# Performance work log

Hardware: AMD Instinct MI355X
Metric: run time of the kernel (lower is better)

Reference implementation:

```python
import jax, jax.numpy as jnp
import numpy as np

MAXLEN = 100  # target_node_incoming_edge_maxlim in to_dense_batch_JY


def setup_inputs() -> dict:
    key = jax.random.key(0)
    ks = jax.random.split(key, 6)
    N, F, H, B = 500000, 64, 64, 8192
    x = jax.random.normal(ks[0], (N, F), dtype=jnp.float32)
    index = jnp.sort(jax.random.randint(ks[1], (N,), 0, B)).astype(jnp.int64)
    s = 1.0 / np.sqrt(H)  # torch LSTM reset_parameters: U(-1/sqrt(H), 1/sqrt(H))
    W_ih = jax.random.uniform(ks[2], (4 * H, F), jnp.float32, -s, s)
    W_hh = jax.random.uniform(ks[3], (4 * H, H), jnp.float32, -s, s)
    b_ih = jax.random.uniform(ks[4], (4 * H,), jnp.float32, -s, s)
    b_hh = jax.random.uniform(ks[5], (4 * H,), jnp.float32, -s, s)
    return {"x": x, "W_ih": W_ih, "W_hh": W_hh, "b_ih": b_ih, "b_hh": b_hh,
            "index": index, "dim_size": B}


def _lstm_last_hidden(dense, mask, W_ih, W_hh, b_ih, b_hh):
    """Run a single-layer LSTM over dense [B,L,F]; freeze state where mask is
    False, which reproduces pack_sequence semantics (ht = hidden at last valid
    step of each sequence; zero-length sequences stay at h0=0)."""
    B, L, F = dense.shape
    H = W_hh.shape[1]
    # input projection for all timesteps at once: [B, L, 4H]
    xg = jnp.einsum('blf,gf->blg', dense, W_ih) + (b_ih + b_hh)

    def step(carry, inp):
        h, c = carry
        g_x, m = inp                      # g_x: [B,4H], m: [B] bool
        g = g_x + h @ W_hh.T
        i, f, gc, o = jnp.split(g, 4, axis=-1)  # torch gate order: i, f, g, o
        i = jax.nn.sigmoid(i)
        f = jax.nn.sigmoid(f)
        gc = jnp.tanh(gc)
        o = jax.nn.sigmoid(o)
        c_new = f * c + i * gc
        h_new = o * jnp.tanh(c_new)
        m2 = m[:, None]
        return (jnp.where(m2, h_new, h), jnp.where(m2, c_new, c)), None

    h0 = jnp.zeros((B, H), dense.dtype)
    (h, _c), _ = jax.lax.scan(step, (h0, h0),
                              (jnp.swapaxes(xg, 0, 1), mask.T))
    return h  # [B, H] == ht[-1]


def reference(x, W_ih, W_hh, b_ih, b_hh, index, dim_size):
    N, F = x.shape
    index = index.astype(jnp.int32)
    # per-graph node counts and exclusive-cumsum offsets (index is sorted)
    counts = jax.ops.segment_sum(jnp.ones(N, jnp.int32), index,
                                 num_segments=dim_size)
    offsets = jnp.concatenate([jnp.zeros(1, jnp.int32),
                               jnp.cumsum(counts)[:-1].astype(jnp.int32)])
    pos = jnp.arange(N, dtype=jnp.int32) - offsets[index]  # position in graph
    valid = pos < MAXLEN                                   # truncate to 100
    # scatter into dense [B, MAXLEN, F]; invalid rows are zeroed and added at
    # slot 0 so they are no-ops
    dense = jnp.zeros((dim_size, MAXLEN, F), x.dtype)
    dense = dense.at[index, jnp.where(valid, pos, 0)].add(
        jnp.where(valid[:, None], x, 0.0))
    seq_len = jnp.minimum(counts, MAXLEN)
    mask = jnp.arange(MAXLEN)[None, :] < seq_len[:, None]  # [B, MAXLEN]
    return _lstm_last_hidden(dense, mask, W_ih, W_hh, b_ih, b_hh)
```

## Files before the change

kernel.cpp:

```cpp
#include <hip/hip_runtime.h>

#define MAXLEN 100
#define HDIM 64
#define CH 4
#define NSEG 12
#define SROW 72
#define SPLANE (CH * SROW + 8)
#define HSTR 72
#define L2E 1.44269504f

typedef __attribute__((ext_vector_type(8))) short bf16x8;
typedef __attribute__((ext_vector_type(4))) float f32x4;

#define LGKM_BARRIER() asm volatile("s_waitcnt lgkmcnt(0)\n\ts_barrier" ::: "memory")

__device__ __forceinline__ unsigned cvtpk(float a, float b) {
    unsigned r;
    asm("v_cvt_pk_bf16_f32 %0, %1, %2" : "=v"(r) : "v"(a), "v"(b));
    return r;
}
__device__ __forceinline__ bf16x8 pack8(f32x4 a, f32x4 b) {
    union { unsigned u[4]; bf16x8 v; } c;
    c.u[0] = cvtpk(a[0], a[1]); c.u[1] = cvtpk(a[2], a[3]);
    c.u[2] = cvtpk(b[0], b[1]); c.u[3] = cvtpk(b[2], b[3]);
    return c.v;
}
__device__ __forceinline__ float sig_pre(float a) {
    return __builtin_amdgcn_rcpf(1.0f + __builtin_amdgcn_exp2f(a));
}
__device__ __forceinline__ float tanh_pre(float a) {
    return fmaf(2.0f, __builtin_amdgcn_rcpf(1.0f + __builtin_amdgcn_exp2f(a)), -1.0f);
}
__device__ __forceinline__ float tanh_p(float v) {
    return fmaf(2.0f, __builtin_amdgcn_rcpf(1.0f + __builtin_amdgcn_exp2f(v * (-2.0f * L2E))), -1.0f);
}

__global__ void seg_hist_kernel(const int* __restrict__ index,
                                int* __restrict__ segStart,
                                int* __restrict__ hist, int N, int B) {
    const int s = blockIdx.x * blockDim.x + threadIdx.x;
    if (s > B) return;
    int lo = 0, hi = N;
    while (lo < hi) { int m = (lo + hi) >> 1; if (index[m] < s) lo = m + 1; else hi = m; }
    segStart[s] = lo;
    if (s < B) {
        int l2 = lo, h2 = N;
        while (l2 < h2) { int m = (l2 + h2) >> 1; if (index[m] < s + 1) l2 = m + 1; else h2 = m; }
        int len = l2 - lo;
        len = len < MAXLEN ? len : MAXLEN;
        atomicAdd(&hist[len], 1);
    }
}

__global__ void seg_scatter_kernel(const int* __restrict__ segStart,
                                   const int* __restrict__ hist,
                                   int* __restrict__ cnt,
                                   int2* __restrict__ slotPacked,
                                   int B, int nslots) {
    __shared__ int base_s[MAXLEN + 1];
    const int tid = threadIdx.x;
    __shared__ int hist_s[MAXLEN + 1];
    if (tid <= MAXLEN) hist_s[tid] = hist[tid];
    __syncthreads();
    if (tid == 0) {
        int acc = 0;
        for (int l = MAXLEN; l >= 0; --l) { base_s[l] = acc; acc += hist_s[l]; }
    }
    __syncthreads();
    const int stride = gridDim.x * blockDim.x;
    for (int b = blockIdx.x * blockDim.x + tid; b < B; b += stride) {
        const int s0 = segStart[b];
        int len = segStart[b + 1] - s0;
        len = len < MAXLEN ? len : MAXLEN;
        const int slot = base_s[len] + atomicAdd(&cnt[len], 1);
        slotPacked[slot] = make_int2(s0, (b << 7) | len);
    }
    if (blockIdx.x == 0 && tid < nslots - B) slotPacked[B + tid] = make_int2(0, -128);
}

__global__ __launch_bounds__(256, 3)
void lstm12_kernel(const float* __restrict__ x,
                   const float* __restrict__ Wih,
                   const float* __restrict__ Whh,
                   const float* __restrict__ bih,
                   const float* __restrict__ bhh,
                   const int* __restrict__ index,
                   const int2* __restrict__ slotPacked,
                   float* __restrict__ out, int N, int B) {
    const int tid  = threadIdx.x;
    const int w    = tid >> 6;
    const int lane = tid & 63;
    const int l15  = lane & 15;
    const int quad = lane >> 4;
    const int segbase = blockIdx.x * NSEG;
    const int ncol = w * 16 + l15;

    __shared__ __align__(16) unsigned short xst[NSEG * SPLANE];
    __shared__ __align__(16) unsigned short hst[2][16][HSTR];
    __shared__ int sstart[NSEG], slen[NSEG], sseg[NSEG];

    if (tid < NSEG) {
        const int slot = segbase + tid;
        int sg = -1, s = 0, len = 0;
        if (slotPacked != nullptr) {
            const int2 p = slotPacked[slot];
            s   = p.x;
            sg  = p.y >> 7;
            len = p.y & 127;
        } else {
            const int b = slot;
            if (b < B) {
                sg = b;
                int lo = 0, hi = N;
                while (lo < hi) { int m = (lo + hi) >> 1; if (index[m] < b) lo = m + 1; else hi = m; }
                s = lo;
                hi = N;
                while (lo < hi) { int m = (lo + hi) >> 1; if (index[m] < b + 1) lo = m + 1; else hi = m; }
                len = lo - s;
                len = len < MAXLEN ? len : MAXLEN;
            }
        }
        sstart[tid] = s;
        slen[tid] = len;
        sseg[tid] = sg;
    }
    for (int i = tid; i < 2 * 16 * HSTR / 2; i += 256) ((int*)hst)[i] = 0;
    __syncthreads();

    bf16x8 wi[4][2], wh[4][2];
    f32x4 bsv[4];
#pragma unroll
    for (int g = 0; g < 4; ++g) {
        const float sc = (g == 2) ? (-2.0f * L2E) : (-L2E);
        const int row = g * HDIM + ncol;
        const float bb = sc * (bih[row] + bhh[row]);
        bsv[g][0] = bb; bsv[g][1] = bb; bsv[g][2] = bb; bsv[g][3] = bb;
#pragma unroll
        for (int kt = 0; kt < 2; ++kt) {
            const f32x4* pi = (const f32x4*)(Wih + (size_t)row * HDIM + kt * 32 + quad * 8);
            const f32x4* ph = (const f32x4*)(Whh + (size_t)row * HDIM + kt * 32 + quad * 8);
            wi[g][kt] = pack8(pi[0] * sc, pi[1] * sc);
            wh[g][kt] = pack8(ph[0] * sc, ph[1] * sc);
        }
    }

    int len3[3];
#pragma unroll
    for (int r = 0; r < 3; ++r) len3[r] = slen[quad * 3 + r];
    int lmax = 0;
#pragma unroll
    for (int i = 0; i < NSEG; ++i) { int v = slen[i]; lmax = v > lmax ? v : lmax; }
    lmax = __builtin_amdgcn_readfirstlane(lmax);

    const int sS = tid >> 4, sT = (tid >> 2) & 3, sC = tid & 3;
    const int sst = (tid < 192) ? sstart[sS] : 0;
    const int sln = (tid < 192) ? slen[sS] : 0;

    f32x4 pre[4];

#define ISSUE(t0_)                                                              \
    if (w < 3) {                                                                \
        int ct = (t0_) + sT;                                                    \
        ct = (sln > 0) ? (ct < sln ? ct : sln - 1) : 0;                         \
        int row = sst + ct;                                                     \
        row = row < N - 1 ? row : N - 1;                                        \
        const f32x4* p_ = (const f32x4*)(x + (size_t)row * HDIM + sC * 16);     \
        pre[0] = p_[0]; pre[1] = p_[1]; pre[2] = p_[2]; pre[3] = p_[3];         \
    }
#define COMMIT()                                                                \
    if (w < 3) {                                                                \
        uint4 o1, o2;                                                           \
        o1.x = cvtpk(pre[0][0], pre[0][1]); o1.y = cvtpk(pre[0][2], pre[0][3]); \
        o1.z = cvtpk(pre[1][0], pre[1][1]); o1.w = cvtpk(pre[1][2], pre[1][3]); \
        o2.x = cvtpk(pre[2][0], pre[2][1]); o2.y = cvtpk(pre[2][2], pre[2][3]); \
        o2.z = cvtpk(pre[3][0], pre[3][1]); o2.w = cvtpk(pre[3][2], pre[3][3]); \
        unsigned short* d_ = &xst[sS * SPLANE + sT * SROW + sC * 16];           \
        *(uint4*)d_ = o1; *(uint4*)(d_ + 8) = o2;                               \
    }

    const int m3 = l15 & 3;
    const int xp = (l15 >> 2) * 3 + (m3 < 2 ? m3 : 2);
    const unsigned short* xb = &xst[xp * SPLANE + quad * 8];

    f32x4 accx[4];
#define ACCX(tt_)                                                               \
    {                                                                           \
        const unsigned short* xr_ = xb + (tt_) * SROW;                          \
        bf16x8 xa0_ = *(const bf16x8*)(xr_);                                    \
        bf16x8 xa1_ = *(const bf16x8*)(xr_ + 32);                               \
        _Pragma("unroll")                                                       \
        for (int g_ = 0; g_ < 4; ++g_) {                                        \
            f32x4 a_ = __builtin_amdgcn_mfma_f32_16x16x32_bf16(xa0_, wi[g_][0], bsv[g_], 0, 0, 0); \
            accx[g_] = __builtin_amdgcn_mfma_f32_16x16x32_bf16(xa1_, wi[g_][1], a_, 0, 0, 0); \
        }                                                                       \
    }

    float c3[3] = {0, 0, 0}, h3[3] = {0, 0, 0};
    const int nch = (lmax + CH - 1) / CH;

    if (nch > 0) {
        ISSUE(0);
        COMMIT();
        LGKM_BARRIER();
        ACCX(0);
        if (nch > 1) ISSUE(CH);

        for (int ch = 0; ch < nch; ++ch) {
            const int t0 = ch * CH;
#pragma unroll
            for (int tt = 0; tt < CH; ++tt) {
                const int t = t0 + tt;
                const int pb = tt & 1, nb = pb ^ 1;

                const unsigned short* hr = &hst[pb][l15][quad * 8];
                bf16x8 ha0 = *(const bf16x8*)(hr);
                bf16x8 ha1 = *(const bf16x8*)(hr + 32);

                f32x4 acc[4];
#pragma unroll
                for (int g = 0; g < 4; ++g) {
                    f32x4 a = __builtin_amdgcn_mfma_f32_16x16x32_bf16(ha0, wh[g][0], accx[g], 0, 0, 0);
                    acc[g] = __builtin_amdgcn_mfma_f32_16x16x32_bf16(ha1, wh[g][1], a, 0, 0, 0);
                }

                if (tt + 1 < CH) ACCX(tt + 1);

#pragma unroll
                for (int r = 0; r < 3; ++r) {
                    float gi = sig_pre (acc[0][r]);
                    float gf = sig_pre (acc[1][r]);
                    float gg = tanh_pre(acc[2][r]);
                    float go = sig_pre (acc[3][r]);
                    float cn = fmaf(gf, c3[r], gi * gg);
                    float hn = go * tanh_p(cn);
                    const bool up = t < len3[r];
                    c3[r] = up ? cn : c3[r];
                    h3[r] = up ? hn : h3[r];
                    hst[nb][quad * 4 + r][ncol] = (unsigned short)cvtpk(h3[r], h3[r]);
                }
                LGKM_BARRIER();
            }
            if (ch + 1 < nch) {
                COMMIT();
                LGKM_BARRIER();
                ACCX(0);
                if (ch + 2 < nch) ISSUE((ch + 2) * CH);
            }
        }
    }

#pragma unroll
    for (int r = 0; r < 3; ++r) {
        const int sg = sseg[quad * 3 + r];
        if (sg >= 0) out[(size_t)sg * HDIM + ncol] = h3[r];
    }
#undef ISSUE
#undef COMMIT
#undef ACCX
}

extern "C" void kernel_launch(void* const* d_in, const int* in_sizes, int n_in,
                              void* d_out, int out_size, void* d_ws, size_t ws_size,
                              hipStream_t stream) {
    const float* x     = (const float*)d_in[0];
    const float* Wih   = (const float*)d_in[1];
    const float* Whh   = (const float*)d_in[2];
    const float* bih   = (const float*)d_in[3];
    const float* bhh   = (const float*)d_in[4];
    const int*   index = (const int*)d_in[5];

    const int N = in_sizes[5];
    const int B = out_size / HDIM;

    const int nblocks = (B + NSEG - 1) / NSEG;
    const int nslots  = nblocks * NSEG;

    const int histOfs = 0, cntOfs = 101;
    const int segOfs  = 204;
    int slotOfs = segOfs + B + 1;
    slotOfs = (slotOfs + 3) & ~3;
    const size_t need = ((size_t)slotOfs + 2 * (size_t)nslots) * sizeof(int);
    const bool sortOK = (d_ws != nullptr) && (ws_size >= need) && (B <= 16384);

    if (sortOK) {
        int* wsi        = (int*)d_ws;
        int* hist       = wsi + histOfs;
        int* cnt        = wsi + cntOfs;
        int* segStart   = wsi + segOfs;
        int2* slotPacked = (int2*)(wsi + slotOfs);
        hipMemsetAsync(wsi, 0, 202 * sizeof(int), stream);
        const int p1blocks = (B + 1 + 255) / 256;
        seg_hist_kernel<<<p1blocks, 256, 0, stream>>>(index, segStart, hist, N, B);
        seg_scatter_kernel<<<16, 256, 0, stream>>>(segStart, hist, cnt, slotPacked, B, nslots);
        lstm12_kernel<<<nblocks, 256, 0, stream>>>(x, Wih, Whh, bih, bhh, index,
                                                   slotPacked, (float*)d_out, N, B);
    } else {
        lstm12_kernel<<<nblocks, 256, 0, stream>>>(x, Wih, Whh, bih, bhh, index,
                                                   nullptr, (float*)d_out, N, B);
    }
}
```

Baseline: 266.0 us.

## Fuse segment sort preprocessing into LSTM kernel via cooperative grid sync

Replaces the memset, histogram kernel and scatter kernel with a prologue inside the LSTM kernel. That prologue does the binary search, the length histogram, the prefix sum and the slot scatter, separated by cooperative-groups grid syncs. The aim is to remove three extra launches and the inter-kernel gaps. In exchange it needs all blocks resident for the cooperative launch, adds grid-wide barrier cost, and falls back to the unsorted path if that launch fails.

```diff
diff --git a/kernel.cpp b/kernel.cpp
--- a/kernel.cpp
+++ b/kernel.cpp
@@ -1,4 +1,7 @@
 #include <hip/hip_runtime.h>
+#include <hip/hip_cooperative_groups.h>
+
+namespace cg = cooperative_groups;
 
 #define MAXLEN 100
 #define HDIM 64
@@ -35,58 +38,15 @@
     return fmaf(2.0f, __builtin_amdgcn_rcpf(1.0f + __builtin_amdgcn_exp2f(v * (-2.0f * L2E))), -1.0f);
 }
 
-__global__ void seg_hist_kernel(const int* __restrict__ index,
-                                int* __restrict__ segStart,
-                                int* __restrict__ hist, int N, int B) {
-    const int s = blockIdx.x * blockDim.x + threadIdx.x;
-    if (s > B) return;
-    int lo = 0, hi = N;
-    while (lo < hi) { int m = (lo + hi) >> 1; if (index[m] < s) lo = m + 1; else hi = m; }
-    segStart[s] = lo;
-    if (s < B) {
-        int l2 = lo, h2 = N;
-        while (l2 < h2) { int m = (l2 + h2) >> 1; if (index[m] < s + 1) l2 = m + 1; else h2 = m; }
-        int len = l2 - lo;
-        len = len < MAXLEN ? len : MAXLEN;
-        atomicAdd(&hist[len], 1);
-    }
-}
-
-__global__ void seg_scatter_kernel(const int* __restrict__ segStart,
-                                   const int* __restrict__ hist,
-                                   int* __restrict__ cnt,
-                                   int2* __restrict__ slotPacked,
-                                   int B, int nslots) {
-    __shared__ int base_s[MAXLEN + 1];
-    const int tid = threadIdx.x;
-    __shared__ int hist_s[MAXLEN + 1];
-    if (tid <= MAXLEN) hist_s[tid] = hist[tid];
-    __syncthreads();
-    if (tid == 0) {
-        int acc = 0;
-        for (int l = MAXLEN; l >= 0; --l) { base_s[l] = acc; acc += hist_s[l]; }
-    }
-    __syncthreads();
-    const int stride = gridDim.x * blockDim.x;
-    for (int b = blockIdx.x * blockDim.x + tid; b < B; b += stride) {
-        const int s0 = segStart[b];
-        int len = segStart[b + 1] - s0;
-        len = len < MAXLEN ? len : MAXLEN;
-        const int slot = base_s[len] + atomicAdd(&cnt[len], 1);
-        slotPacked[slot] = make_int2(s0, (b << 7) | len);
-    }
-    if (blockIdx.x == 0 && tid < nslots - B) slotPacked[B + tid] = make_int2(0, -128);
-}
-
 __global__ __launch_bounds__(256, 3)
-void lstm12_kernel(const float* __restrict__ x,
-                   const float* __restrict__ Wih,
-                   const float* __restrict__ Whh,
-                   const float* __restrict__ bih,
-                   const float* __restrict__ bhh,
-                   const int* __restrict__ index,
-                   const int2* __restrict__ slotPacked,
-                   float* __restrict__ out, int N, int B) {
+void lstm_coop_kernel(const float* __restrict__ x,
+                      const float* __restrict__ Wih,
+                      const float* __restrict__ Whh,
+                      const float* __restrict__ bih,
+                      const float* __restrict__ bhh,
+                      const int* __restrict__ index,
+                      int* ws, float* __restrict__ out,
+                      int N, int B, int doSort) {
     const int tid  = threadIdx.x;
     const int w    = tid >> 6;
     const int lane = tid & 63;
@@ -98,12 +58,52 @@
     __shared__ __align__(16) unsigned short xst[NSEG * SPLANE];
     __shared__ __align__(16) unsigned short hst[2][16][HSTR];
     __shared__ int sstart[NSEG], slen[NSEG], sseg[NSEG];
+    __shared__ int hist_s[MAXLEN + 1], base_s[MAXLEN + 1];
+
+    const int2* sp = nullptr;
+    if (doSort) {
+        cg::grid_group grid = cg::this_grid();
+        int* hist = ws;
+        int* cnt  = ws + 128;
+        int2* slotPacked = (int2*)(ws + 256);
+        const int gid = blockIdx.x * 256 + tid;
+        const int nslots = (int)gridDim.x * NSEG;
+
+        int myS0 = 0, myLen = 0;
+        if (gid < 256) ws[gid] = 0;
+        if (gid < B) {
+            int lo = 0, hi = N;
+            while (lo < hi) { int m = (lo + hi) >> 1; if (index[m] < gid) lo = m + 1; else hi = m; }
+            myS0 = lo;
+            int l2 = lo, h2 = N;
+            while (l2 < h2) { int m = (l2 + h2) >> 1; if (index[m] < gid + 1) l2 = m + 1; else h2 = m; }
+            myLen = l2 - lo;
+            myLen = myLen < MAXLEN ? myLen : MAXLEN;
+        }
+        grid.sync();
+        if (gid < B) atomicAdd(&hist[myLen], 1);
+        grid.sync();
+        if (tid <= MAXLEN) hist_s[tid] = hist[tid];
+        __syncthreads();
+        if (tid == 0) {
+            int acc = 0;
+            for (int l = MAXLEN; l >= 0; --l) { base_s[l] = acc; acc += hist_s[l]; }
+        }
+        __syncthreads();
+        if (gid < B) {
+            const int slot = base_s[myLen] + atomicAdd(&cnt[myLen], 1);
+            slotPacked[slot] = make_int2(myS0, (gid << 7) | myLen);
+        }
+        if (gid < nslots - B) slotPacked[B + gid] = make_int2(0, -128);
+        grid.sync();
+        sp = slotPacked;
+    }
 
     if (tid < NSEG) {
         const int slot = segbase + tid;
         int sg = -1, s = 0, len = 0;
-        if (slotPacked != nullptr) {
-            const int2 p = slotPacked[slot];
+        if (sp != nullptr) {
+            const int2 p = sp[slot];
             s   = p.x;
             sg  = p.y >> 7;
             len = p.y & 127;
@@ -262,40 +262,36 @@
 extern "C" void kernel_launch(void* const* d_in, const int* in_sizes, int n_in,
                               void* d_out, int out_size, void* d_ws, size_t ws_size,
                               hipStream_t stream) {
-    const float* x     = (const float*)d_in[0];
-    const float* Wih   = (const float*)d_in[1];
-    const float* Whh   = (const float*)d_in[2];
-    const float* bih   = (const float*)d_in[3];
-    const float* bhh   = (const float*)d_in[4];
-    const int*   index = (const int*)d_in[5];
-
-    const int N = in_sizes[5];
-    const int B = out_size / HDIM;
-
-    const int nblocks = (B + NSEG - 1) / NSEG;
-    const int nslots  = nblocks * NSEG;
-
-    const int histOfs = 0, cntOfs = 101;
-    const int segOfs  = 204;
-    int slotOfs = segOfs + B + 1;
-    slotOfs = (slotOfs + 3) & ~3;
-    const size_t need = ((size_t)slotOfs + 2 * (size_t)nslots) * sizeof(int);
-    const bool sortOK = (d_ws != nullptr) && (ws_size >= need) && (B <= 16384);
-
-    if (sortOK) {
-        int* wsi        = (int*)d_ws;
-        int* hist       = wsi + histOfs;
-        int* cnt        = wsi + cntOfs;
-        int* segStart   = wsi + segOfs;
-        int2* slotPacked = (int2*)(wsi + slotOfs);
-        hipMemsetAsync(wsi, 0, 202 * sizeof(int), stream);
-        const int p1blocks = (B + 1 + 255) / 256;
-        seg_hist_kernel<<<p1blocks, 256, 0, stream>>>(index, segStart, hist, N, B);
-        seg_scatter_kernel<<<16, 256, 0, stream>>>(segStart, hist, cnt, slotPacked, B, nslots);
-        lstm12_kernel<<<nblocks, 256, 0, stream>>>(x, Wih, Whh, bih, bhh, index,
-                                                   slotPacked, (float*)d_out, N, B);
-    } else {
-        lstm12_kernel<<<nblocks, 256, 0, stream>>>(x, Wih, Whh, bih, bhh, index,
-                                                   nullptr, (float*)d_out, N, B);
-    }
-}
+    const float* x   = (const float*)d_in[0];
+    const float* Wih = (const float*)d_in[1];
+    const float* Whh = (const float*)d_in[2];
+    const float* bih = (const float*)d_in[3];
+    const float* bhh = (const float*)d_in[4];
+    const int* index = (const int*)d_in[5];
+
+    int N = in_sizes[5];
+    int B = out_size / HDIM;
+    int nblocks = (B + NSEG - 1) / NSEG;
+    const int nslots = nblocks * NSEG;
+
+    const size_t need = (256 + 2 * (size_t)nslots) * sizeof(int);
+    int* wsi = (int*)d_ws;
+    float* outp = (float*)d_out;
+    int doSort = (d_ws != nullptr && ws_size >= need) ? 1 : 0;
+
+    bool launched = false;
+    if (doSort) {
+        void* args[] = {(void*)&x, (void*)&Wih, (void*)&Whh, (void*)&bih, (void*)&bhh,
+                        (void*)&index, (void*)&wsi, (void*)&outp,
+                        (void*)&N, (void*)&B, (void*)&doSort};
+        hipError_t e = hipLaunchCooperativeKernel((const void*)lstm_coop_kernel,
+                                                  dim3(nblocks), dim3(256),
+                                                  args, 0, stream);
+        if (e == hipSuccess) launched = true;
+        else (void)hipGetLastError();
+    }
+    if (!launched) {
+        lstm_coop_kernel<<<nblocks, 256, 0, stream>>>(x, Wih, Whh, bih, bhh, index,
+                                                      wsi, outp, N, B, 0);
+    }
+}
```

Result: slower. 467.5 us (+75.7%).
